# Performance work log

Hardware: AMD Instinct MI355X
Metric: run time of the kernel (lower is better)

Reference implementation:

```python
import jax, jax.numpy as jnp
import numpy as np

N = 2_000_000
NUM_PTS = 500_000
NUM_GROUPS = 10_000
NUM_POSITIONS = 8
NUM_CAMS = 8


def _quat_mul(q1, q2):
    """Hamilton product, quaternions stored [x, y, z, w] (pypose convention)."""
    v1, w1 = q1[..., :3], q1[..., 3:4]
    v2, w2 = q2[..., :3], q2[..., 3:4]
    w = w1 * w2 - jnp.sum(v1 * v2, axis=-1, keepdims=True)
    v = w1 * v2 + w2 * v1 + jnp.cross(v1, v2)
    return jnp.concatenate([v, w], axis=-1)


def _quat_rotate(q, p):
    """Rotate points p [...,3] by unit quaternion q [...,4] ([x,y,z,w])."""
    v, w = q[..., :3], q[..., 3:4]
    uv = jnp.cross(v, p)
    uuv = jnp.cross(v, uv)
    return p + 2.0 * (w * uv + uuv)


def _random_se3(key, n, rot_scale=0.1, trans_scale=0.5):
    kq, kt = jax.random.split(key)
    qv = rot_scale * jax.random.normal(kq, (n, 3), dtype=jnp.float32)
    qw = jnp.ones((n, 1), dtype=jnp.float32)
    q = jnp.concatenate([qv, qw], axis=-1)
    q = q / jnp.linalg.norm(q, axis=-1, keepdims=True)
    t = trans_scale * jax.random.normal(kt, (n, 3), dtype=jnp.float32)
    return jnp.concatenate([t, q], axis=-1)  # [n,7] = [tx,ty,tz,qx,qy,qz,qw]


def setup_inputs() -> dict:
    key = jax.random.key(0)
    ks = jax.random.split(key, 10)
    points_2d = 1000.0 * jax.random.uniform(ks[0], (N, 2), dtype=jnp.float32)
    camera_indices = jax.random.randint(ks[1], (N,), 0, NUM_CAMS)
    group_idx = jax.random.randint(ks[2], (N,), 0, NUM_GROUPS)
    member_idx = jax.random.randint(ks[3], (N,), 0, NUM_POSITIONS)
    grouping_indices = jnp.stack([group_idx, member_idx], axis=-1)  # [N,2]
    point_indices = jax.random.randint(ks[4], (N,), 0, NUM_PTS)
    camera_pps = 500.0 + 10.0 * jax.random.normal(ks[5], (NUM_CAMS, 2), dtype=jnp.float32)
    intrs = 1000.0 + 50.0 * jax.random.normal(ks[6], (NUM_CAMS, 2), dtype=jnp.float32)
    # 3D points in front of the rig: z in [4, 10) to keep projection well-conditioned
    xy = 2.0 * jax.random.normal(ks[7], (NUM_PTS, 2), dtype=jnp.float32)
    z = 4.0 + 6.0 * jax.random.uniform(ks[8], (NUM_PTS, 1), dtype=jnp.float32)
    points_3d = jnp.concatenate([xy, z], axis=-1)
    kref, krel = jax.random.split(ks[9])
    ref_poses = _random_se3(kref, NUM_GROUPS)
    rel_poses = _random_se3(krel, NUM_POSITIONS, rot_scale=0.05, trans_scale=0.2)
    return {
        "points_2d": points_2d,
        "camera_indices": camera_indices,
        "grouping_indices": grouping_indices,
        "point_indices": point_indices,
        "camera_pps": camera_pps,
        "intrs": intrs,
        "points_3d": points_3d,
        "ref_poses": ref_poses,
        "rel_poses": rel_poses,
    }


def reference(points_2d, camera_indices, grouping_indices, point_indices,
              camera_pps, intrs, points_3d, ref_poses, rel_poses):
    group_idx = grouping_indices[:, 0]
    member_idx = grouping_indices[:, 1]
    ref = ref_poses[group_idx]    # [N,7]
    rel = rel_poses[member_idx]   # [N,7]
    # SE3 compose: image_pose = rel @ ref  ->  (t_rel + R_rel * t_ref, q_rel * q_ref)
    t = rel[:, :3] + _quat_rotate(rel[:, 3:], ref[:, :3])
    q = _quat_mul(rel[:, 3:], ref[:, 3:])
    # Transform points into camera frame and project (pinhole)
    p_cam = _quat_rotate(q, points_3d[point_indices]) + t  # [N,3]
    uv = intrs[camera_indices] * (p_cam[:, :2] / p_cam[:, 2:3]) + camera_pps[camera_indices]
    return uv - points_2d  # [N,2] reprojection residual
```

## Files before the change

kernel.cpp:

```cpp
#include <hip/hip_runtime.h>


__global__ __launch_bounds__(256) void reproj_kernel(
    const float2* __restrict__ points_2d,
    const int*    __restrict__ camera_indices,
    const int2*   __restrict__ grouping_indices,
    const int*    __restrict__ point_indices,
    const float*  __restrict__ camera_pps,
    const float*  __restrict__ intrs,
    const float*  __restrict__ points_3d,
    const float*  __restrict__ ref_poses,
    const float*  __restrict__ rel_poses,
    float2*       __restrict__ out,
    int n)
{
    __shared__ float s_rel[56];
    __shared__ float s_pps[16];
    __shared__ float s_intr[16];
    int tid = threadIdx.x;
    if (tid < 56) s_rel[tid] = rel_poses[tid];
    if (tid < 16) { s_pps[tid] = camera_pps[tid]; s_intr[tid] = intrs[tid]; }
    __syncthreads();

    int i = blockIdx.x * blockDim.x + tid;
    if (i >= n) return;

    int2  gm  = grouping_indices[i];
    int   pi  = point_indices[i];
    int   cam = camera_indices[i];
    float2 p2d = points_2d[i];

    const float* rp = ref_poses + 7 * gm.x;
    float rtx = rp[0], rty = rp[1], rtz = rp[2];
    float rqx = rp[3], rqy = rp[4], rqz = rp[5], rqw = rp[6];

    const float* lp = s_rel + 7 * gm.y;
    float ltx = lp[0], lty = lp[1], ltz = lp[2];
    float lqx = lp[3], lqy = lp[4], lqz = lp[5], lqw = lp[6];

    float uvx = lqy * rtz - lqz * rty;
    float uvy = lqz * rtx - lqx * rtz;
    float uvz = lqx * rty - lqy * rtx;
    float uuvx = lqy * uvz - lqz * uvy;
    float uuvy = lqz * uvx - lqx * uvz;
    float uuvz = lqx * uvy - lqy * uvx;
    float tx = ltx + rtx + 2.0f * (lqw * uvx + uuvx);
    float ty = lty + rty + 2.0f * (lqw * uvy + uuvy);
    float tz = ltz + rtz + 2.0f * (lqw * uvz + uuvz);

    float qw = lqw * rqw - (lqx * rqx + lqy * rqy + lqz * rqz);
    float qx = lqw * rqx + rqw * lqx + (lqy * rqz - lqz * rqy);
    float qy = lqw * rqy + rqw * lqy + (lqz * rqx - lqx * rqz);
    float qz = lqw * rqz + rqw * lqz + (lqx * rqy - lqy * rqx);

    const float* pp = points_3d + 3 * pi;
    float px = pp[0], py = pp[1], pz = pp[2];

    float v2x = qy * pz - qz * py;
    float v2y = qz * px - qx * pz;
    float v2z = qx * py - qy * px;
    float w2x = qy * v2z - qz * v2y;
    float w2y = qz * v2x - qx * v2z;
    float w2z = qx * v2y - qy * v2x;
    float pcx = px + 2.0f * (qw * v2x + w2x) + tx;
    float pcy = py + 2.0f * (qw * v2y + w2y) + ty;
    float pcz = pz + 2.0f * (qw * v2z + w2z) + tz;

    float invz = 1.0f / pcz;
    float ux = s_intr[2 * cam]     * (pcx * invz) + s_pps[2 * cam];
    float uy = s_intr[2 * cam + 1] * (pcy * invz) + s_pps[2 * cam + 1];

    out[i] = make_float2(ux - p2d.x, uy - p2d.y);
}

extern "C" void kernel_launch(void* const* d_in, const int* in_sizes, int n_in,
                              void* d_out, int out_size, void* d_ws, size_t ws_size,
                              hipStream_t stream) {
    const float2* points_2d       = (const float2*)d_in[0];
    const int*    camera_indices  = (const int*)d_in[1];
    const int2*   grouping        = (const int2*)d_in[2];
    const int*    point_indices   = (const int*)d_in[3];
    const float*  camera_pps      = (const float*)d_in[4];
    const float*  intrs           = (const float*)d_in[5];
    const float*  points_3d       = (const float*)d_in[6];
    const float*  ref_poses       = (const float*)d_in[7];
    const float*  rel_poses       = (const float*)d_in[8];
    float2*       out             = (float2*)d_out;

    int n = in_sizes[1];
    int blocks = (n + 255) / 256;
    reproj_kernel<<<blocks, 256, 0, stream>>>(
        points_2d, camera_indices, grouping, point_indices,
        camera_pps, intrs, points_3d, ref_poses, rel_poses, out, n);
}
```

Baseline: 128.8 us.

## Repack gathered tables to aligned float4 and process two elements per thread

Adds a pre-pass kernel that copies the 3D points and reference poses into 16-byte-aligned float4 layouts in workspace, so the main kernel can gather them with single vector loads instead of several scalar loads. Each thread in the main kernel now handles two observations, reading the streaming inputs and writing the output with 128-bit nontemporal accesses. The repack adds a second launch and about 8MB of extra traffic every call, and it hardcodes the point and group counts. When no workspace is provided the kernel falls back to the old scalar gathers.

```diff
diff --git a/kernel.cpp b/kernel.cpp
--- a/kernel.cpp
+++ b/kernel.cpp
@@ -1,40 +1,42 @@
 #include <hip/hip_runtime.h>
 
 
-__global__ __launch_bounds__(256) void reproj_kernel(
-    const float2* __restrict__ points_2d,
-    const int*    __restrict__ camera_indices,
-    const int2*   __restrict__ grouping_indices,
-    const int*    __restrict__ point_indices,
-    const float*  __restrict__ camera_pps,
-    const float*  __restrict__ intrs,
-    const float*  __restrict__ points_3d,
-    const float*  __restrict__ ref_poses,
-    const float*  __restrict__ rel_poses,
-    float2*       __restrict__ out,
-    int n)
+typedef float f4 __attribute__((ext_vector_type(4)));
+typedef float f2 __attribute__((ext_vector_type(2)));
+typedef int   i4 __attribute__((ext_vector_type(4)));
+typedef int   i2 __attribute__((ext_vector_type(2)));
+
+enum { NPTS = 500000, NGRP = 10000 };
+
+__global__ __launch_bounds__(256) void repack_kernel(
+    const float* __restrict__ points_3d,
+    const float* __restrict__ ref_poses,
+    f4* __restrict__ ws_pts,
+    f4* __restrict__ ws_ref)
 {
-    __shared__ float s_rel[56];
-    __shared__ float s_pps[16];
-    __shared__ float s_intr[16];
-    int tid = threadIdx.x;
-    if (tid < 56) s_rel[tid] = rel_poses[tid];
-    if (tid < 16) { s_pps[tid] = camera_pps[tid]; s_intr[tid] = intrs[tid]; }
-    __syncthreads();
+    int i = blockIdx.x * blockDim.x + threadIdx.x;
+    if (i < NPTS) {
+        const float* p = points_3d + 3 * i;
+        f4 v; v.x = p[0]; v.y = p[1]; v.z = p[2]; v.w = 0.0f;
+        ws_pts[i] = v;
+    } else if (i < NPTS + NGRP) {
+        int j = i - NPTS;
+        const float* r = ref_poses + 7 * j;
+        f4 a; a.x = r[0]; a.y = r[1]; a.z = r[2]; a.w = r[3];
+        f4 b; b.x = r[4]; b.y = r[5]; b.z = r[6]; b.w = 0.0f;
+        ws_ref[2 * j]     = a;
+        ws_ref[2 * j + 1] = b;
+    }
+}
 
-    int i = blockIdx.x * blockDim.x + tid;
-    if (i >= n) return;
+__device__ __forceinline__ f2 project_one(
+    f4 ra, f4 rb, int m, int cam, f4 P, f2 p2d,
+    const float* s_rel, const float* s_pps, const float* s_intr)
+{
+    float rtx = ra.x, rty = ra.y, rtz = ra.z;
+    float rqx = ra.w, rqy = rb.x, rqz = rb.y, rqw = rb.z;
 
-    int2  gm  = grouping_indices[i];
-    int   pi  = point_indices[i];
-    int   cam = camera_indices[i];
-    float2 p2d = points_2d[i];
-
-    const float* rp = ref_poses + 7 * gm.x;
-    float rtx = rp[0], rty = rp[1], rtz = rp[2];
-    float rqx = rp[3], rqy = rp[4], rqz = rp[5], rqw = rp[6];
-
-    const float* lp = s_rel + 7 * gm.y;
+    const float* lp = s_rel + 7 * m;
     float ltx = lp[0], lty = lp[1], ltz = lp[2];
     float lqx = lp[3], lqy = lp[4], lqz = lp[5], lqw = lp[6];
 
@@ -53,9 +55,7 @@
     float qy = lqw * rqy + rqw * lqy + (lqz * rqx - lqx * rqz);
     float qz = lqw * rqz + rqw * lqz + (lqx * rqy - lqy * rqx);
 
-    const float* pp = points_3d + 3 * pi;
-    float px = pp[0], py = pp[1], pz = pp[2];
-
+    float px = P.x, py = P.y, pz = P.z;
     float v2x = qy * pz - qz * py;
     float v2y = qz * px - qx * pz;
     float v2z = qx * py - qy * px;
@@ -67,10 +67,93 @@
     float pcz = pz + 2.0f * (qw * v2z + w2z) + tz;
 
     float invz = 1.0f / pcz;
-    float ux = s_intr[2 * cam]     * (pcx * invz) + s_pps[2 * cam];
-    float uy = s_intr[2 * cam + 1] * (pcy * invz) + s_pps[2 * cam + 1];
+    f2 r;
+    r.x = s_intr[2 * cam]     * (pcx * invz) + s_pps[2 * cam]     - p2d.x;
+    r.y = s_intr[2 * cam + 1] * (pcy * invz) + s_pps[2 * cam + 1] - p2d.y;
+    return r;
+}
 
-    out[i] = make_float2(ux - p2d.x, uy - p2d.y);
+template<bool REPACK>
+__global__ __launch_bounds__(256) void reproj2_kernel(
+    const float2* __restrict__ points_2d,
+    const int*    __restrict__ camera_indices,
+    const int2*   __restrict__ grouping_indices,
+    const int*    __restrict__ point_indices,
+    const float*  __restrict__ camera_pps,
+    const float*  __restrict__ intrs,
+    const float*  __restrict__ points_3d,
+    const float*  __restrict__ ref_poses,
+    const float*  __restrict__ rel_poses,
+    const f4*     __restrict__ ws_pts,
+    const f4*     __restrict__ ws_ref,
+    float2*       __restrict__ out,
+    int n)
+{
+    __shared__ float s_rel[56];
+    __shared__ float s_pps[16];
+    __shared__ float s_intr[16];
+    int tid = threadIdx.x;
+    if (tid < 56) s_rel[tid] = rel_poses[tid];
+    if (tid < 16) { s_pps[tid] = camera_pps[tid]; s_intr[tid] = intrs[tid]; }
+    __syncthreads();
+
+    int t = blockIdx.x * blockDim.x + tid;
+    int i = 2 * t;
+    if (i >= n) return;
+
+    if (i + 1 < n) {
+        f4 p2 = __builtin_nontemporal_load((const f4*)points_2d + t);
+        i4 gm = __builtin_nontemporal_load((const i4*)grouping_indices + t);
+        i2 pi = __builtin_nontemporal_load((const i2*)point_indices + t);
+        i2 cm = __builtin_nontemporal_load((const i2*)camera_indices + t);
+
+        f4 ra0, rb0, ra1, rb1, P0, P1;
+        if (REPACK) {
+            ra0 = ws_ref[2 * gm.x];  rb0 = ws_ref[2 * gm.x + 1];
+            ra1 = ws_ref[2 * gm.z];  rb1 = ws_ref[2 * gm.z + 1];
+            P0  = ws_pts[pi.x];      P1  = ws_pts[pi.y];
+        } else {
+            const float* rp0 = ref_poses + 7 * gm.x;
+            const float* rp1 = ref_poses + 7 * gm.z;
+            const float* pp0 = points_3d + 3 * pi.x;
+            const float* pp1 = points_3d + 3 * pi.y;
+            ra0.x = rp0[0]; ra0.y = rp0[1]; ra0.z = rp0[2]; ra0.w = rp0[3];
+            rb0.x = rp0[4]; rb0.y = rp0[5]; rb0.z = rp0[6]; rb0.w = 0.0f;
+            ra1.x = rp1[0]; ra1.y = rp1[1]; ra1.z = rp1[2]; ra1.w = rp1[3];
+            rb1.x = rp1[4]; rb1.y = rp1[5]; rb1.z = rp1[6]; rb1.w = 0.0f;
+            P0.x = pp0[0]; P0.y = pp0[1]; P0.z = pp0[2]; P0.w = 0.0f;
+            P1.x = pp1[0]; P1.y = pp1[1]; P1.z = pp1[2]; P1.w = 0.0f;
+        }
+
+        f2 d0, d1;
+        d0.x = p2.x; d0.y = p2.y;
+        d1.x = p2.z; d1.y = p2.w;
+        f2 r0 = project_one(ra0, rb0, gm.y, cm.x, P0, d0, s_rel, s_pps, s_intr);
+        f2 r1 = project_one(ra1, rb1, gm.w, cm.y, P1, d1, s_rel, s_pps, s_intr);
+
+        f4 o; o.x = r0.x; o.y = r0.y; o.z = r1.x; o.w = r1.y;
+        __builtin_nontemporal_store(o, (f4*)out + t);
+    } else {
+        float2 p2d = points_2d[i];
+        int2   gm  = grouping_indices[i];
+        int    pi  = point_indices[i];
+        int    cam = camera_indices[i];
+
+        f4 ra, rb, P;
+        if (REPACK) {
+            ra = ws_ref[2 * gm.x]; rb = ws_ref[2 * gm.x + 1];
+            P  = ws_pts[pi];
+        } else {
+            const float* rp = ref_poses + 7 * gm.x;
+            const float* pp = points_3d + 3 * pi;
+            ra.x = rp[0]; ra.y = rp[1]; ra.z = rp[2]; ra.w = rp[3];
+            rb.x = rp[4]; rb.y = rp[5]; rb.z = rp[6]; rb.w = 0.0f;
+            P.x = pp[0]; P.y = pp[1]; P.z = pp[2]; P.w = 0.0f;
+        }
+        f2 d; d.x = p2d.x; d.y = p2d.y;
+        f2 r = project_one(ra, rb, gm.y, cam, P, d, s_rel, s_pps, s_intr);
+        out[i] = make_float2(r.x, r.y);
+    }
 }
 
 extern "C" void kernel_launch(void* const* d_in, const int* in_sizes, int n_in,
@@ -88,8 +171,24 @@
     float2*       out             = (float2*)d_out;
 
     int n = in_sizes[1];
-    int blocks = (n + 255) / 256;
-    reproj_kernel<<<blocks, 256, 0, stream>>>(
-        points_2d, camera_indices, grouping, point_indices,
-        camera_pps, intrs, points_3d, ref_poses, rel_poses, out, n);
+    int pair_threads = (n + 1) / 2;
+    int blocks = (pair_threads + 255) / 256;
+
+    size_t need = (size_t)NPTS * 16 + (size_t)NGRP * 32;
+    if (d_ws && ws_size >= need) {
+        f4* ws_pts = (f4*)d_ws;
+        f4* ws_ref = (f4*)((char*)d_ws + (size_t)NPTS * 16);
+        int rthreads = NPTS + NGRP;
+        repack_kernel<<<(rthreads + 255) / 256, 256, 0, stream>>>(
+            points_3d, ref_poses, ws_pts, ws_ref);
+        reproj2_kernel<true><<<blocks, 256, 0, stream>>>(
+            points_2d, camera_indices, grouping, point_indices,
+            camera_pps, intrs, points_3d, ref_poses, rel_poses,
+            ws_pts, ws_ref, out, n);
+    } else {
+        reproj2_kernel<false><<<blocks, 256, 0, stream>>>(
+            points_2d, camera_indices, grouping, point_indices,
+            camera_pps, intrs, points_3d, ref_poses, rel_poses,
+            nullptr, nullptr, out, n);
+    }
 }
```

New measurement: 135.7 us. 1.05x slower.

## Process four observations per thread with vectorized nontemporal loads and stores

Applied to the files above, without the earlier changes.

Each thread now handles four consecutive residuals, reading the streaming inputs as 16-byte vectors with nontemporal hints and writing results as two float4 nontemporal stores. Pose gathers are packed into two unaligned 4-wide loads, and point gathers into one 2-wide load plus a scalar. The aim is fewer memory instructions and more gathers in flight per thread. In exchange there are four times fewer threads and higher register pressure, which can cut occupancy and latency hiding for the random gathers.

```diff
diff --git a/kernel.cpp b/kernel.cpp
--- a/kernel.cpp
+++ b/kernel.cpp
@@ -1,7 +1,57 @@
 #include <hip/hip_runtime.h>
 
 
-__global__ __launch_bounds__(256) void reproj_kernel(
+typedef float f4  __attribute__((ext_vector_type(4)));
+typedef float f2  __attribute__((ext_vector_type(2)));
+typedef int   i4  __attribute__((ext_vector_type(4)));
+typedef float f4u __attribute__((ext_vector_type(4), aligned(4)));
+typedef float f2u __attribute__((ext_vector_type(2), aligned(4)));
+
+__device__ __forceinline__ f2 project_one(
+    f4u ra, f4u rb, float px, float py, float pz,
+    int m, int cam, float p2x, float p2y,
+    const float* s_rel, const float* s_pps, const float* s_intr)
+{
+    float rtx = ra.x, rty = ra.y, rtz = ra.z;
+    float rqx = rb.x, rqy = rb.y, rqz = rb.z, rqw = rb.w;
+
+    const float* lp = s_rel + 7 * m;
+    float ltx = lp[0], lty = lp[1], ltz = lp[2];
+    float lqx = lp[3], lqy = lp[4], lqz = lp[5], lqw = lp[6];
+
+    float uvx = lqy * rtz - lqz * rty;
+    float uvy = lqz * rtx - lqx * rtz;
+    float uvz = lqx * rty - lqy * rtx;
+    float uuvx = lqy * uvz - lqz * uvy;
+    float uuvy = lqz * uvx - lqx * uvz;
+    float uuvz = lqx * uvy - lqy * uvx;
+    float tx = ltx + rtx + 2.0f * (lqw * uvx + uuvx);
+    float ty = lty + rty + 2.0f * (lqw * uvy + uuvy);
+    float tz = ltz + rtz + 2.0f * (lqw * uvz + uuvz);
+
+    float qw = lqw * rqw - (lqx * rqx + lqy * rqy + lqz * rqz);
+    float qx = lqw * rqx + rqw * lqx + (lqy * rqz - lqz * rqy);
+    float qy = lqw * rqy + rqw * lqy + (lqz * rqx - lqx * rqz);
+    float qz = lqw * rqz + rqw * lqz + (lqx * rqy - lqy * rqx);
+
+    float v2x = qy * pz - qz * py;
+    float v2y = qz * px - qx * pz;
+    float v2z = qx * py - qy * px;
+    float w2x = qy * v2z - qz * v2y;
+    float w2y = qz * v2x - qx * v2z;
+    float w2z = qx * v2y - qy * v2x;
+    float pcx = px + 2.0f * (qw * v2x + w2x) + tx;
+    float pcy = py + 2.0f * (qw * v2y + w2y) + ty;
+    float pcz = pz + 2.0f * (qw * v2z + w2z) + tz;
+
+    float invz = 1.0f / pcz;
+    f2 r;
+    r.x = s_intr[2 * cam]     * (pcx * invz) + s_pps[2 * cam]     - p2x;
+    r.y = s_intr[2 * cam + 1] * (pcy * invz) + s_pps[2 * cam + 1] - p2y;
+    return r;
+}
+
+__global__ __launch_bounds__(256) void reproj4_kernel(
     const float2* __restrict__ points_2d,
     const int*    __restrict__ camera_indices,
     const int2*   __restrict__ grouping_indices,
@@ -22,55 +72,68 @@
     if (tid < 16) { s_pps[tid] = camera_pps[tid]; s_intr[tid] = intrs[tid]; }
     __syncthreads();
 
-    int i = blockIdx.x * blockDim.x + tid;
+    int t = blockIdx.x * blockDim.x + tid;
+    int i = 4 * t;
     if (i >= n) return;
 
-    int2  gm  = grouping_indices[i];
-    int   pi  = point_indices[i];
-    int   cam = camera_indices[i];
-    float2 p2d = points_2d[i];
+    if (i + 3 < n) {
+        f4 p2a = __builtin_nontemporal_load((const f4*)points_2d + 2 * t);
+        f4 p2b = __builtin_nontemporal_load((const f4*)points_2d + 2 * t + 1);
+        i4 gma = __builtin_nontemporal_load((const i4*)grouping_indices + 2 * t);
+        i4 gmb = __builtin_nontemporal_load((const i4*)grouping_indices + 2 * t + 1);
+        i4 pi  = __builtin_nontemporal_load((const i4*)point_indices + t);
+        i4 cm  = __builtin_nontemporal_load((const i4*)camera_indices + t);
 
-    const float* rp = ref_poses + 7 * gm.x;
-    float rtx = rp[0], rty = rp[1], rtz = rp[2];
-    float rqx = rp[3], rqy = rp[4], rqz = rp[5], rqw = rp[6];
+        const float* rp0 = ref_poses + 7 * gma.x;
+        const float* rp1 = ref_poses + 7 * gma.z;
+        const float* rp2 = ref_poses + 7 * gmb.x;
+        const float* rp3 = ref_poses + 7 * gmb.z;
+        f4u ra0 = *(const f4u*)rp0;
+        f4u rb0 = *(const f4u*)(rp0 + 3);
+        f4u ra1 = *(const f4u*)rp1;
+        f4u rb1 = *(const f4u*)(rp1 + 3);
+        f4u ra2 = *(const f4u*)rp2;
+        f4u rb2 = *(const f4u*)(rp2 + 3);
+        f4u ra3 = *(const f4u*)rp3;
+        f4u rb3 = *(const f4u*)(rp3 + 3);
 
-    const float* lp = s_rel + 7 * gm.y;
-    float ltx = lp[0], lty = lp[1], ltz = lp[2];
-    float lqx = lp[3], lqy = lp[4], lqz = lp[5], lqw = lp[6];
+        const float* pp0 = points_3d + 3 * pi.x;
+        const float* pp1 = points_3d + 3 * pi.y;
+        const float* pp2 = points_3d + 3 * pi.z;
+        const float* pp3 = points_3d + 3 * pi.w;
+        f2u P0 = *(const f2u*)pp0; float pz0 = pp0[2];
+        f2u P1 = *(const f2u*)pp1; float pz1 = pp1[2];
+        f2u P2 = *(const f2u*)pp2; float pz2 = pp2[2];
+        f2u P3 = *(const f2u*)pp3; float pz3 = pp3[2];
 
-    float uvx = lqy * rtz - lqz * rty;
-    float uvy = lqz * rtx - lqx * rtz;
-    float uvz = lqx * rty - lqy * rtx;
-    float uuvx = lqy * uvz - lqz * uvy;
-    float uuvy = lqz * uvx - lqx * uvz;
-    float uuvz = lqx * uvy - lqy * uvx;
-    float tx = ltx + rtx + 2.0f * (lqw * uvx + uuvx);
-    float ty = lty + rty + 2.0f * (lqw * uvy + uuvy);
-    float tz = ltz + rtz + 2.0f * (lqw * uvz + uuvz);
+        f2 r0 = project_one(ra0, rb0, P0.x, P0.y, pz0, gma.y, cm.x,
+                            p2a.x, p2a.y, s_rel, s_pps, s_intr);
+        f2 r1 = project_one(ra1, rb1, P1.x, P1.y, pz1, gma.w, cm.y,
+                            p2a.z, p2a.w, s_rel, s_pps, s_intr);
+        f2 r2 = project_one(ra2, rb2, P2.x, P2.y, pz2, gmb.y, cm.z,
+                            p2b.x, p2b.y, s_rel, s_pps, s_intr);
+        f2 r3 = project_one(ra3, rb3, P3.x, P3.y, pz3, gmb.w, cm.w,
+                            p2b.z, p2b.w, s_rel, s_pps, s_intr);
 
-    float qw = lqw * rqw - (lqx * rqx + lqy * rqy + lqz * rqz);
-    float qx = lqw * rqx + rqw * lqx + (lqy * rqz - lqz * rqy);
-    float qy = lqw * rqy + rqw * lqy + (lqz * rqx - lqx * rqz);
-    float qz = lqw * rqz + rqw * lqz + (lqx * rqy - lqy * rqx);
-
-    const float* pp = points_3d + 3 * pi;
-    float px = pp[0], py = pp[1], pz = pp[2];
-
-    float v2x = qy * pz - qz * py;
-    float v2y = qz * px - qx * pz;
-    float v2z = qx * py - qy * px;
-    float w2x = qy * v2z - qz * v2y;
-    float w2y = qz * v2x - qx * v2z;
-    float w2z = qx * v2y - qy * v2x;
-    float pcx = px + 2.0f * (qw * v2x + w2x) + tx;
-    float pcy = py + 2.0f * (qw * v2y + w2y) + ty;
-    float pcz = pz + 2.0f * (qw * v2z + w2z) + tz;
-
-    float invz = 1.0f / pcz;
-    float ux = s_intr[2 * cam]     * (pcx * invz) + s_pps[2 * cam];
-    float uy = s_intr[2 * cam + 1] * (pcy * invz) + s_pps[2 * cam + 1];
-
-    out[i] = make_float2(ux - p2d.x, uy - p2d.y);
+        f4 oa; oa.x = r0.x; oa.y = r0.y; oa.z = r1.x; oa.w = r1.y;
+        f4 ob; ob.x = r2.x; ob.y = r2.y; ob.z = r3.x; ob.w = r3.y;
+        __builtin_nontemporal_store(oa, (f4*)out + 2 * t);
+        __builtin_nontemporal_store(ob, (f4*)out + 2 * t + 1);
+    } else {
+        for (int k = i; k < n; ++k) {
+            float2 p2d = points_2d[k];
+            int2   gm  = grouping_indices[k];
+            int    pik = point_indices[k];
+            int    cam = camera_indices[k];
+            const float* rp = ref_poses + 7 * gm.x;
+            f4u ra = *(const f4u*)rp;
+            f4u rb = *(const f4u*)(rp + 3);
+            const float* pp = points_3d + 3 * pik;
+            f2 r = project_one(ra, rb, pp[0], pp[1], pp[2], gm.y, cam,
+                               p2d.x, p2d.y, s_rel, s_pps, s_intr);
+            out[k] = make_float2(r.x, r.y);
+        }
+    }
 }
 
 extern "C" void kernel_launch(void* const* d_in, const int* in_sizes, int n_in,
@@ -88,8 +151,9 @@
     float2*       out             = (float2*)d_out;
 
     int n = in_sizes[1];
-    int blocks = (n + 255) / 256;
-    reproj_kernel<<<blocks, 256, 0, stream>>>(
+    int threads = (n + 3) / 4;
+    int blocks = (threads + 255) / 256;
+    reproj4_kernel<<<blocks, 256, 0, stream>>>(
         points_2d, camera_indices, grouping, point_indices,
         camera_pps, intrs, points_3d, ref_poses, rel_poses, out, n);
 }
```

Result: slower. 141.2 us (+9.6%).

## Precompute composed group-member poses in a separate kernel and gather them

Applied to the files above, without the earlier changes.

Adds a pre-pass kernel that composes all 10000x8 ref/rel pose pairs into a workspace table of two float4s each. The main kernel then gathers one 32-byte composed pose instead of a 28-byte ref pose plus shared-memory rel pose and the composition math. Streaming inputs and the output now use nontemporal loads and stores. This costs an extra kernel launch and a 2.5 MB table write and read, and it hardcodes the group and position counts. The original inline kernel is kept as a fallback when the workspace is too small.

```diff
diff --git a/kernel.cpp b/kernel.cpp
--- a/kernel.cpp
+++ b/kernel.cpp
@@ -1,7 +1,122 @@
 #include <hip/hip_runtime.h>
 
 
+typedef float f4  __attribute__((ext_vector_type(4)));
+typedef float f2  __attribute__((ext_vector_type(2)));
+typedef float f4u __attribute__((ext_vector_type(4), aligned(4)));
+
+enum { NGRP = 10000, NPOS = 8 };
+
+__global__ __launch_bounds__(256) void compose_kernel(
+    const float* __restrict__ ref_poses,
+    const float* __restrict__ rel_poses,
+    f4* __restrict__ ws)
+{
+    int j = blockIdx.x * blockDim.x + threadIdx.x;
+    if (j >= NGRP * NPOS) return;
+    int g = j >> 3, m = j & 7;
+
+    const float* rp = ref_poses + 7 * g;
+    f4u ra = *(const f4u*)rp;
+    f4u rb = *(const f4u*)(rp + 3);
+    float rtx = ra.x, rty = ra.y, rtz = ra.z;
+    float rqx = rb.x, rqy = rb.y, rqz = rb.z, rqw = rb.w;
+
+    const float* lp = rel_poses + 7 * m;
+    float ltx = lp[0], lty = lp[1], ltz = lp[2];
+    float lqx = lp[3], lqy = lp[4], lqz = lp[5], lqw = lp[6];
+
+    float uvx = lqy * rtz - lqz * rty;
+    float uvy = lqz * rtx - lqx * rtz;
+    float uvz = lqx * rty - lqy * rtx;
+    float uuvx = lqy * uvz - lqz * uvy;
+    float uuvy = lqz * uvx - lqx * uvz;
+    float uuvz = lqx * uvy - lqy * uvx;
+    float tx = ltx + rtx + 2.0f * (lqw * uvx + uuvx);
+    float ty = lty + rty + 2.0f * (lqw * uvy + uuvy);
+    float tz = ltz + rtz + 2.0f * (lqw * uvz + uuvz);
+
+    float qw = lqw * rqw - (lqx * rqx + lqy * rqy + lqz * rqz);
+    float qx = lqw * rqx + rqw * lqx + (lqy * rqz - lqz * rqy);
+    float qy = lqw * rqy + rqw * lqy + (lqz * rqx - lqx * rqz);
+    float qz = lqw * rqz + rqw * lqz + (lqx * rqy - lqy * rqx);
+
+    f4 a; a.x = tx; a.y = ty; a.z = tz; a.w = qx;
+    f4 b; b.x = qy; b.y = qz; b.z = qw; b.w = 0.0f;
+    ws[2 * j]     = a;
+    ws[2 * j + 1] = b;
+}
+
+__device__ __forceinline__ f2 project_composed(
+    f4 ca, f4 cb, float px, float py, float pz,
+    int cam, float p2x, float p2y,
+    const float* s_pps, const float* s_intr)
+{
+    float tx = ca.x, ty = ca.y, tz = ca.z;
+    float qx = ca.w, qy = cb.x, qz = cb.y, qw = cb.z;
+
+    float v2x = qy * pz - qz * py;
+    float v2y = qz * px - qx * pz;
+    float v2z = qx * py - qy * px;
+    float w2x = qy * v2z - qz * v2y;
+    float w2y = qz * v2x - qx * v2z;
+    float w2z = qx * v2y - qy * v2x;
+    float pcx = px + 2.0f * (qw * v2x + w2x) + tx;
+    float pcy = py + 2.0f * (qw * v2y + w2y) + ty;
+    float pcz = pz + 2.0f * (qw * v2z + w2z) + tz;
+
+    float invz = 1.0f / pcz;
+    f2 r;
+    r.x = s_intr[2 * cam]     * (pcx * invz) + s_pps[2 * cam]     - p2x;
+    r.y = s_intr[2 * cam + 1] * (pcy * invz) + s_pps[2 * cam + 1] - p2y;
+    return r;
+}
+
 __global__ __launch_bounds__(256) void reproj_kernel(
+    const float2* __restrict__ points_2d,
+    const int*    __restrict__ camera_indices,
+    const int2*   __restrict__ grouping_indices,
+    const int*    __restrict__ point_indices,
+    const float*  __restrict__ camera_pps,
+    const float*  __restrict__ intrs,
+    const float*  __restrict__ points_3d,
+    const f4*     __restrict__ composed,
+    float2*       __restrict__ out,
+    int n)
+{
+    __shared__ float s_pps[16];
+    __shared__ float s_intr[16];
+    int tid = threadIdx.x;
+    if (tid < 16) { s_pps[tid] = camera_pps[tid]; s_intr[tid] = intrs[tid]; }
+    __syncthreads();
+
+    int i = blockIdx.x * blockDim.x + tid;
+    if (i >= n) return;
+
+    float2 p2d;
+    { f2 v = __builtin_nontemporal_load((const f2*)points_2d + i);
+      p2d.x = v.x; p2d.y = v.y; }
+    int2 gm;
+    { typedef int i2v __attribute__((ext_vector_type(2)));
+      i2v v = __builtin_nontemporal_load((const i2v*)grouping_indices + i);
+      gm.x = v.x; gm.y = v.y; }
+    int pi  = __builtin_nontemporal_load(point_indices + i);
+    int cam = __builtin_nontemporal_load(camera_indices + i);
+
+    int c = 8 * gm.x + gm.y;
+    f4 ca = composed[2 * c];
+    f4 cb = composed[2 * c + 1];
+
+    const float* pp = points_3d + 3 * pi;
+    float px = pp[0], py = pp[1], pz = pp[2];
+
+    f2 r = project_composed(ca, cb, px, py, pz, cam, p2d.x, p2d.y,
+                            s_pps, s_intr);
+    f2 o; o.x = r.x; o.y = r.y;
+    __builtin_nontemporal_store(o, (f2*)out + i);
+}
+
+__global__ __launch_bounds__(256) void reproj_inline_kernel(
     const float2* __restrict__ points_2d,
     const int*    __restrict__ camera_indices,
     const int2*   __restrict__ grouping_indices,
@@ -33,7 +148,6 @@
     const float* rp = ref_poses + 7 * gm.x;
     float rtx = rp[0], rty = rp[1], rtz = rp[2];
     float rqx = rp[3], rqy = rp[4], rqz = rp[5], rqw = rp[6];
-
     const float* lp = s_rel + 7 * gm.y;
     float ltx = lp[0], lty = lp[1], ltz = lp[2];
     float lqx = lp[3], lqy = lp[4], lqz = lp[5], lqw = lp[6];
@@ -56,21 +170,11 @@
     const float* pp = points_3d + 3 * pi;
     float px = pp[0], py = pp[1], pz = pp[2];
 
-    float v2x = qy * pz - qz * py;
-    float v2y = qz * px - qx * pz;
-    float v2z = qx * py - qy * px;
-    float w2x = qy * v2z - qz * v2y;
-    float w2y = qz * v2x - qx * v2z;
-    float w2z = qx * v2y - qy * v2x;
-    float pcx = px + 2.0f * (qw * v2x + w2x) + tx;
-    float pcy = py + 2.0f * (qw * v2y + w2y) + ty;
-    float pcz = pz + 2.0f * (qw * v2z + w2z) + tz;
-
-    float invz = 1.0f / pcz;
-    float ux = s_intr[2 * cam]     * (pcx * invz) + s_pps[2 * cam];
-    float uy = s_intr[2 * cam + 1] * (pcy * invz) + s_pps[2 * cam + 1];
-
-    out[i] = make_float2(ux - p2d.x, uy - p2d.y);
+    f4 ca; ca.x = tx; ca.y = ty; ca.z = tz; ca.w = qx;
+    f4 cb; cb.x = qy; cb.y = qz; cb.z = qw; cb.w = 0.0f;
+    f2 r = project_composed(ca, cb, px, py, pz, cam, p2d.x, p2d.y,
+                            s_pps, s_intr);
+    out[i] = make_float2(r.x, r.y);
 }
 
 extern "C" void kernel_launch(void* const* d_in, const int* in_sizes, int n_in,
@@ -89,7 +193,19 @@
 
     int n = in_sizes[1];
     int blocks = (n + 255) / 256;
-    reproj_kernel<<<blocks, 256, 0, stream>>>(
-        points_2d, camera_indices, grouping, point_indices,
-        camera_pps, intrs, points_3d, ref_poses, rel_poses, out, n);
-}
+
+    size_t need = (size_t)NGRP * NPOS * 32;
+    if (d_ws && ws_size >= need) {
+        f4* ws = (f4*)d_ws;
+        int cthreads = NGRP * NPOS;
+        compose_kernel<<<(cthreads + 255) / 256, 256, 0, stream>>>(
+            ref_poses, rel_poses, ws);
+        reproj_kernel<<<blocks, 256, 0, stream>>>(
+            points_2d, camera_indices, grouping, point_indices,
+            camera_pps, intrs, points_3d, ws, out, n);
+    } else {
+        reproj_inline_kernel<<<blocks, 256, 0, stream>>>(
+            points_2d, camera_indices, grouping, point_indices,
+            camera_pps, intrs, points_3d, ref_poses, rel_poses, out, n);
+    }
+}
```

Measured after the change: 141.0 us. +9.5%, slower.
